# Performance work log

Measured on AMD Instinct MI355X. Metric: run time of the kernel, lower is better.

## Reference

```python
import jax, jax.numpy as jnp
import numpy as np
import math

B, TU, TM, D, H = 4, 2048, 256, 1024, 16
DH = D // H
PAIRS = D // 2
LAM = 0.7
EPS_PHASE = 1e-8


def balance_norm(x, w, b, bal_w):
    mu = x.mean(-1, keepdims=True)
    var = ((x - mu) ** 2).mean(-1, keepdims=True)
    normed = (x - mu) / jnp.sqrt(var + 1e-6) * w + b
    half = x.shape[-1] // 2
    e1 = (x[..., :half] ** 2).mean(-1, keepdims=True)
    e2 = (x[..., half:] ** 2).mean(-1, keepdims=True)
    imb = (e1 - e2) * bal_w  # (B,T,1)
    corr = jnp.concatenate([
        jnp.broadcast_to(-imb, x[..., :half].shape),
        jnp.broadcast_to(imb, x[..., half:].shape)], axis=-1)
    return normed + corr


def phase_resonance(a, b):
    # a: (B,Tq,D), b: (B,Tk,D). mean_p cos(th_a - th_b) == (cosA@cosB^T + sinA@sinB^T)/pairs
    def to_phase(x):
        x2 = x.reshape(*x.shape[:-1], PAIRS, 2)
        return jnp.arctan2(x2[..., 1] + EPS_PHASE, x2[..., 0] + EPS_PHASE)
    ta, tb = to_phase(a), to_phase(b)
    ca, sa = jnp.cos(ta), jnp.sin(ta)
    cb, sb = jnp.cos(tb), jnp.sin(tb)
    r = (jnp.einsum('bqp,bkp->bqk', ca, cb) + jnp.einsum('bqp,bkp->bqk', sa, sb)) / PAIRS
    return r


def mha(q_in, kv_in, wq, wk, wv, wo, a_gate, e_gate):
    Bq, Tq, _ = q_in.shape
    Tk = kv_in.shape[1]
    q = (q_in @ wq.T).reshape(Bq, Tq, H, DH)
    k = (kv_in @ wk.T).reshape(Bq, Tk, H, DH)
    v = (kv_in @ wv.T).reshape(Bq, Tk, H, DH)
    scores = jnp.einsum('bqhd,bkhd->bhqk', q, k) / math.sqrt(DH)
    attn = jax.nn.softmax(scores, axis=-1)
    ag = a_gate[:, None, :, :]              # (B,1,Tq,1)
    eg = jnp.swapaxes(e_gate[:, None], 2, 3)  # (B,1,1,Tk)
    attn = attn * ag * eg
    attn = attn / (attn.sum(-1, keepdims=True) + 1e-8)
    ctx = jnp.einsum('bhqk,bkhd->bqhd', attn, v).reshape(Bq, Tq, D)
    return ctx @ wo.T


def setup_inputs() -> dict:
    key = jax.random.key(0)
    ks = jax.random.split(key, 16)
    s = 0.02
    return {
        'o_micro': jax.random.normal(ks[0], (B, TU, D), jnp.float32),
        'o_macro': jax.random.normal(ks[1], (B, TM, D), jnp.float32),
        'r_conv_acc': jax.random.normal(ks[2], (B, TM, TU), jnp.float32) * 0.1,
        'r_emer_acc': jax.random.normal(ks[3], (B, TU, TM), jnp.float32) * 0.1,
        'ln_u_w': jnp.ones((D,), jnp.float32),
        'ln_u_b': jnp.zeros((D,), jnp.float32),
        'bw_u': jnp.float32(0.01),
        'ln_m_w': jnp.ones((D,), jnp.float32),
        'ln_m_b': jnp.zeros((D,), jnp.float32),
        'bw_m': jnp.float32(0.01),
        'gu_w': jax.random.normal(ks[4], (1, D), jnp.float32) * s,
        'gu_b': jnp.zeros((1,), jnp.float32),
        'gm_w': jax.random.normal(ks[5], (1, D), jnp.float32) * s,
        'gm_b': jnp.zeros((1,), jnp.float32),
        'conv_q_w': jax.random.normal(ks[6], (D, D), jnp.float32) * s,
        'conv_k_w': jax.random.normal(ks[7], (D, D), jnp.float32) * s,
        'conv_v_w': jax.random.normal(ks[8], (D, D), jnp.float32) * s,
        'conv_out_w': jax.random.normal(ks[9], (D, D), jnp.float32) * s,
        'emer_q_w': jax.random.normal(ks[10], (D, D), jnp.float32) * s,
        'emer_k_w': jax.random.normal(ks[11], (D, D), jnp.float32) * s,
        'emer_v_w': jax.random.normal(ks[12], (D, D), jnp.float32) * s,
        'emer_out_w': jax.random.normal(ks[13], (D, D), jnp.float32) * s,
        'res_alpha': jnp.float32(1.0),
    }


def reference(o_micro, o_macro, r_conv_acc, r_emer_acc,
              ln_u_w, ln_u_b, bw_u, ln_m_w, ln_m_b, bw_m,
              gu_w, gu_b, gm_w, gm_b,
              conv_q_w, conv_k_w, conv_v_w, conv_out_w,
              emer_q_w, emer_k_w, emer_v_w, emer_out_w, res_alpha):
    ou = balance_norm(o_micro, ln_u_w, ln_u_b, bw_u)
    om = balance_norm(o_macro, ln_m_w, ln_m_b, bw_m)
    g_micro = jax.nn.sigmoid(ou @ gu_w.T + gu_b)  # (B,Tu,1)
    g_macro = jax.nn.sigmoid(om @ gm_w.T + gm_b)  # (B,Tm,1)
    r_conv_inst = phase_resonance(om, ou)  # (B,Tm,Tu)
    r_emer_inst = phase_resonance(ou, om)  # (B,Tu,Tm)
    r_conv_new = LAM * r_conv_acc + (1 - LAM) * r_conv_inst
    r_emer_new = LAM * r_emer_acc + (1 - LAM) * r_emer_inst
    r_conv_scalar = jax.nn.sigmoid(res_alpha * r_conv_new.mean(-1, keepdims=True))
    r_emer_scalar = jax.nn.sigmoid(res_alpha * r_emer_new.mean(-1, keepdims=True))
    delta_macro = mha(om, ou, conv_q_w, conv_k_w, conv_v_w, conv_out_w, g_macro, g_micro)
    o_macro_new = o_macro + delta_macro * r_conv_scalar
    delta_micro = mha(ou, om, emer_q_w, emer_k_w, emer_v_w, emer_out_w, g_micro, g_macro)
    o_micro_new = o_micro + delta_micro * r_emer_scalar
    return (o_micro_new, o_macro_new, r_conv_new, r_emer_new)
```

## Files before the change

### kernel.cpp

```cpp
#include <hip/hip_runtime.h>
#include <math.h>

typedef unsigned short u16;
typedef __attribute__((ext_vector_type(8))) short bf16x8;
typedef __attribute__((ext_vector_type(4))) float f32x4;

__device__ __forceinline__ float sigmoidf_(float x) { return 1.0f / (1.0f + __expf(-x)); }
__device__ __forceinline__ u16 f2bf(float v) {
    union { float f; unsigned u; } x; x.f = v;
    unsigned r = x.u + 0x7fffu + ((x.u >> 16) & 1u);
    return (u16)(r >> 16);
}
__device__ __forceinline__ float bf2f(u16 u) {
    union { unsigned u; float f; } x; x.u = ((unsigned)u) << 16; return x.f;
}

#define GLD(src, dst) __builtin_amdgcn_global_load_lds( \
        (const __attribute__((address_space(1))) void*)(src), \
        (__attribute__((address_space(3))) void*)(dst), 16, 0, 0)
#define GLD4(src, dst) __builtin_amdgcn_global_load_lds( \
        (const __attribute__((address_space(1))) void*)(src), \
        (__attribute__((address_space(3))) void*)(dst), 4, 0, 0)

__global__ void __launch_bounds__(256) norm_gate_kernel(
    const float* __restrict__ X,
    const float* __restrict__ w, const float* __restrict__ bvec,
    const float* __restrict__ bw_p,
    const float* __restrict__ gw, const float* __restrict__ gb_p,
    u16* __restrict__ OUT, u16* __restrict__ PN, float* __restrict__ G)
{
    const int row = blockIdx.x * 4 + (threadIdx.x >> 6);
    const int lane = threadIdx.x & 63;
    const float* xr = X + (size_t)row * 1024 + lane * 16;
    float4 xa = ((const float4*)xr)[0];
    float4 xb = ((const float4*)xr)[1];
    float4 xc = ((const float4*)xr)[2];
    float4 xd = ((const float4*)xr)[3];
    float s1 = (xa.x + xa.y + xa.z + xa.w) + (xb.x + xb.y + xb.z + xb.w)
             + (xc.x + xc.y + xc.z + xc.w) + (xd.x + xd.y + xd.z + xd.w);
    float s2 = xa.x * xa.x + xa.y * xa.y + xa.z * xa.z + xa.w * xa.w
             + xb.x * xb.x + xb.y * xb.y + xb.z * xb.z + xb.w * xb.w
             + xc.x * xc.x + xc.y * xc.y + xc.z * xc.z + xc.w * xc.w
             + xd.x * xd.x + xd.y * xd.y + xd.z * xd.z + xd.w * xd.w;
    #pragma unroll
    for (int o = 1; o <= 32; o <<= 1) s1 += __shfl_xor(s1, o);
    float h2 = s2;
    #pragma unroll
    for (int o = 1; o <= 16; o <<= 1) h2 += __shfl_xor(h2, o);
    const float oth = __shfl_xor(h2, 32);
    const float slo = (lane < 32) ? h2 : oth;
    const float shi = (lane < 32) ? oth : h2;
    const float mu = s1 * (1.0f / 1024.0f);
    const float var = (slo + shi) * (1.0f / 1024.0f) - mu * mu;
    const float rstd = rsqrtf(var + 1e-6f);
    const float imb = (slo - shi) * (1.0f / 512.0f) * (*bw_p);
    const float corr = (lane < 32) ? -imb : imb;
    const int i0 = lane * 16;
    const float4* wp = (const float4*)(w + i0);
    const float4* bp = (const float4*)(bvec + i0);
    const float4* gp = (const float4*)(gw + i0);
    float o16[16];
    float gd = 0.0f;
    #pragma unroll
    for (int q = 0; q < 4; ++q) {
        float4 xv = (q == 0) ? xa : (q == 1) ? xb : (q == 2) ? xc : xd;
        float4 wv = wp[q], bv = bp[q], gv = gp[q];
        float t0 = (xv.x - mu) * rstd * wv.x + bv.x + corr;
        float t1 = (xv.y - mu) * rstd * wv.y + bv.y + corr;
        float t2 = (xv.z - mu) * rstd * wv.z + bv.z + corr;
        float t3 = (xv.w - mu) * rstd * wv.w + bv.w + corr;
        gd += t0 * gv.x + t1 * gv.y + t2 * gv.z + t3 * gv.w;
        o16[4 * q + 0] = t0; o16[4 * q + 1] = t1; o16[4 * q + 2] = t2; o16[4 * q + 3] = t3;
    }
    #pragma unroll
    for (int o = 1; o <= 32; o <<= 1) gd += __shfl_xor(gd, o);
    if (lane == 0) G[row] = sigmoidf_(gd + *gb_p);
    u16 ob[16], pn[16];
    #pragma unroll
    for (int j = 0; j < 16; ++j) ob[j] = f2bf(o16[j]);
    #pragma unroll
    for (int j = 0; j < 8; ++j) {
        float px = o16[2 * j] + 1e-8f, py = o16[2 * j + 1] + 1e-8f;
        float rr = rsqrtf(px * px + py * py);
        pn[2 * j] = f2bf(px * rr); pn[2 * j + 1] = f2bf(py * rr);
    }
    *(uint4*)(OUT + (size_t)row * 1024 + i0) = *(uint4*)ob;
    *(uint4*)(OUT + (size_t)row * 1024 + i0 + 8) = *(uint4*)(ob + 8);
    *(uint4*)(PN + (size_t)row * 1024 + i0) = *(uint4*)pn;
    *(uint4*)(PN + (size_t)row * 1024 + i0 + 8) = *(uint4*)(pn + 8);
}

__global__ void __launch_bounds__(256) wconv_kernel(
    const float* w0, const float* w1, const float* w2, const float* w3,
    const float* w4, const float* w5, const float* w6, const float* w7,
    u16* __restrict__ dst)
{
    const float* s;
    switch (blockIdx.y) {
        case 0: s = w0; break; case 1: s = w1; break;
        case 2: s = w2; break; case 3: s = w3; break;
        case 4: s = w4; break; case 5: s = w5; break;
        case 6: s = w6; break; default: s = w7; break;
    }
    long i = (long)blockIdx.x * 1024 + threadIdx.x * 4;
    float4 v = *(const float4*)(s + i);
    u16 o[4] = { f2bf(v.x), f2bf(v.y), f2bf(v.z), f2bf(v.w) };
    *(uint2*)(dst + (long)blockIdx.y * 1048576 + i) = *(uint2*)o;
}

__global__ void __launch_bounds__(256) attn_flash(
    const u16* __restrict__ Q, const u16* __restrict__ K,
    const u16* __restrict__ VT, const float* __restrict__ AG,
    const float* __restrict__ EG, u16* __restrict__ OC,
    int TQ, int TKV, long vbs)
{
    __shared__ __align__(16) u16 shm[21504];
    float* egf = (float*)(shm + 20480);
    const int t = threadIdx.x;
    const int lane = t & 63, w = t >> 6;
    const int l15 = lane & 15, g = lane >> 4;
    const int qt = blockIdx.x, h = blockIdx.y, b = blockIdx.z;
    const long qrow = (long)b * TQ + qt * 64 + w * 16 + l15;
    const u16* Qp = Q + qrow * 1024 + h * 64 + g * 8;
    const bf16x8 qf0 = *(const bf16x8*)(Qp);
    const bf16x8 qf1 = *(const bf16x8*)(Qp + 32);
    const u16* Kp = K + ((long)b * TKV + w * 16 + l15) * 1024 + h * 64 + g * 8;
    const u16* Vp = VT + (long)b * vbs + (long)(h * 64 + w * 16 + l15) * TKV + g * 8;
    const float* egp = EG + (long)b * TKV + lane;

    auto stage = [&](int kvt, int buf) {
        GLD(Kp + (long)kvt * 1024,      shm + buf * 4096 + (w * 2 + 0) * 512);
        GLD(Kp + (long)kvt * 1024 + 32, shm + buf * 4096 + (w * 2 + 1) * 512);
        GLD(Vp + kvt,      shm + 8192 + buf * 4096 + (w * 2 + 0) * 512);
        GLD(Vp + kvt + 32, shm + 8192 + buf * 4096 + (w * 2 + 1) * 512);
        GLD4(egp + kvt, egf + (buf * 4 + w) * 64);
    };

    const int nT = TKV >> 6;
    f32x4 O[4] = {};
    float mrun = -3.0e38f, lrun = 0.0f, serun = 0.0f;
    stage(0, 0);
    for (int i = 0; i < nT; ++i) {
        const int buf = i & 1;
        if (i + 1 < nT) {
            stage((i + 1) << 6, buf ^ 1);
            asm volatile("s_waitcnt vmcnt(5)" ::: "memory");
        } else {
            asm volatile("s_waitcnt vmcnt(0)" ::: "memory");
        }
        __builtin_amdgcn_sched_barrier(0);
        __builtin_amdgcn_s_barrier();
        const u16* kb = shm + buf * 4096;
        const u16* vb = shm + 8192 + buf * 4096;
        f32x4 sa[4] = {};
        #pragma unroll
        for (int kvf = 0; kvf < 4; ++kvf) {
            bf16x8 kf = *(const bf16x8*)(kb + (kvf * 2 + 0) * 512 + lane * 8);
            sa[kvf] = __builtin_amdgcn_mfma_f32_16x16x32_bf16(kf, qf0, sa[kvf], 0, 0, 0);
        }
        #pragma unroll
        for (int kvf = 0; kvf < 4; ++kvf) {
            bf16x8 kf = *(const bf16x8*)(kb + (kvf * 2 + 1) * 512 + lane * 8);
            sa[kvf] = __builtin_amdgcn_mfma_f32_16x16x32_bf16(kf, qf1, sa[kvf], 0, 0, 0);
        }
        float ev[4][4];
        float tmax = -3.0e38f;
        #pragma unroll
        for (int kvf = 0; kvf < 4; ++kvf)
            #pragma unroll
            for (int j = 0; j < 4; ++j) {
                float s = sa[kvf][j] * 0.125f;
                ev[kvf][j] = s;
                tmax = fmaxf(tmax, s);
            }
        tmax = fmaxf(tmax, __shfl_xor(tmax, 16));
        tmax = fmaxf(tmax, __shfl_xor(tmax, 32));
        const float mnew = fmaxf(mrun, tmax);
        const float corr = __expf(mrun - mnew);
        mrun = mnew;
        float suml = 0.0f, sumg = 0.0f;
        unsigned pk[4][2];
        #pragma unroll
        for (int kvf = 0; kvf < 4; ++kvf) {
            float4 eg4 = *(const float4*)(egf + (buf * 4 + w) * 64 + kvf * 16 + 4 * g);
            float e0 = __expf(ev[kvf][0] - mnew);
            float e1 = __expf(ev[kvf][1] - mnew);
            float e2 = __expf(ev[kvf][2] - mnew);
            float e3 = __expf(ev[kvf][3] - mnew);
            suml += (e0 + e1) + (e2 + e3);
            float g0 = e0 * eg4.x, g1 = e1 * eg4.y, g2 = e2 * eg4.z, g3 = e3 * eg4.w;
            sumg += (g0 + g1) + (g2 + g3);
            pk[kvf][0] = (unsigned)f2bf(g0) | ((unsigned)f2bf(g1) << 16);
            pk[kvf][1] = (unsigned)f2bf(g2) | ((unsigned)f2bf(g3) << 16);
        }
        suml += __shfl_xor(suml, 16); suml += __shfl_xor(suml, 32);
        sumg += __shfl_xor(sumg, 16); sumg += __shfl_xor(sumg, 32);
        lrun = lrun * corr + suml;
        serun = serun * corr + sumg;
        #pragma unroll
        for (int fd = 0; fd < 4; ++fd)
            #pragma unroll
            for (int j = 0; j < 4; ++j) O[fd][j] *= corr;
        u16* pw = shm + 16384 + w * 1024;
        #pragma unroll
        for (int kvf = 0; kvf < 4; ++kvf) {
            const int base = (kvf >> 1) * 512
                           + (l15 + 16 * (2 * (kvf & 1) + (g >> 1))) * 8
                           + 4 * (g & 1);
            *(unsigned*)(pw + base) = pk[kvf][0];
            *(unsigned*)(pw + base + 2) = pk[kvf][1];
        }
        #pragma unroll
        for (int ksv = 0; ksv < 2; ++ksv) {
            bf16x8 pf = *(const bf16x8*)(pw + ksv * 512 + lane * 8);
            #pragma unroll
            for (int fd = 0; fd < 4; ++fd) {
                bf16x8 vf = *(const bf16x8*)(vb + (fd * 2 + ksv) * 512 + lane * 8);
                O[fd] = __builtin_amdgcn_mfma_f32_16x16x32_bf16(vf, pf, O[fd], 0, 0, 0);
            }
        }
        if (i + 1 < nT) __builtin_amdgcn_s_barrier();
    }
    const float agv = AG[qrow];
    const float fac = agv / (agv * serun + lrun * 1e-8f);
    __syncthreads();
    u16* tw = shm + w * 1152;
    #pragma unroll
    for (int fd = 0; fd < 4; ++fd) {
        const int d0 = fd * 16 + 4 * g;
        unsigned v01 = (unsigned)f2bf(O[fd][0] * fac) | ((unsigned)f2bf(O[fd][1] * fac) << 16);
        unsigned v23 = (unsigned)f2bf(O[fd][2] * fac) | ((unsigned)f2bf(O[fd][3] * fac) << 16);
        *(unsigned*)(tw + l15 * 72 + d0) = v01;
        *(unsigned*)(tw + l15 * 72 + d0 + 2) = v23;
    }
    const int qr = lane >> 2, part = lane & 3;
    uint4 va = *(const uint4*)(tw + qr * 72 + part * 16);
    uint4 vb2 = *(const uint4*)(tw + qr * 72 + part * 16 + 8);
    u16* op = OC + ((long)b * TQ + qt * 64 + w * 16 + qr) * 1024 + h * 64 + part * 16;
    *(uint4*)(op) = va;
    *(uint4*)(op + 8) = vb2;
}

#define RD_A(BUF, MQ) do { \
    _Pragma("unroll") for (int fr_ = 0; fr_ < 4; ++fr_) \
    _Pragma("unroll") for (int kk_ = 0; kk_ < 2; ++kk_) \
        af[fr_][kk_] = *(const bf16x8*)(sh + (BUF) * BUFSZ + (MQ) * 8192 + (wm * 4 + fr_) * 1024 + kk_ * 512 + lane * 8); \
} while (0)
#define RD_B(BUF, NQ, DST) do { \
    _Pragma("unroll") for (int fc_ = 0; fc_ < NRC; ++fc_) \
    _Pragma("unroll") for (int kk_ = 0; kk_ < 2; ++kk_) \
        DST[fc_][kk_] = *(const bf16x8*)(sh + (BUF) * BUFSZ + 16384 + (NQ) * BHALF + (wn * NRC + fc_) * 1024 + kk_ * 512 + lane * 8); \
} while (0)
#define MM(SRC, MQ, NQ) do { \
    __builtin_amdgcn_s_setprio(1); \
    _Pragma("unroll") for (int fr_ = 0; fr_ < 4; ++fr_) \
    _Pragma("unroll") for (int fc_ = 0; fc_ < NRC; ++fc_) \
    _Pragma("unroll") for (int kk_ = 0; kk_ < 2; ++kk_) \
        acc[(MQ) * 4 + fr_][(NQ) * NRC + fc_] = __builtin_amdgcn_mfma_f32_16x16x32_bf16( \
            af[fr_][kk_], SRC[fc_][kk_], acc[(MQ) * 4 + fr_][(NQ) * NRC + fc_], 0, 0, 0); \
    __builtin_amdgcn_s_setprio(0); \
} while (0)
#define FENCE1() do { \
    __builtin_amdgcn_s_barrier(); \
    asm volatile("s_waitcnt lgkmcnt(0)" ::: "memory"); \
    __builtin_amdgcn_sched_barrier(0); \
} while (0)
#define FENCE2(VM) do { \
    __builtin_amdgcn_sched_barrier(0); \
    if ((VM) == 1) { \
        if constexpr (BN == 256) asm volatile("s_waitcnt vmcnt(8)" ::: "memory"); \
        else                     asm volatile("s_waitcnt vmcnt(6)" ::: "memory"); \
    } else if ((VM) == 2) { asm volatile("s_waitcnt vmcnt(0)" ::: "memory"); } \
    __builtin_amdgcn_s_barrier(); \
} while (0)

template<int BN, int EPI>
__global__ void __launch_bounds__(512, 1) mfma256(
    const u16* __restrict__ A, const u16* __restrict__ B,
    void* __restrict__ C, void* __restrict__ Cx, void* __restrict__ Cy,
    int K, int lda, int ldb,
    const float* __restrict__ base, const float* __restrict__ rs)
{
    constexpr int NRC = BN / 128;
    constexpr int BHALF = BN * 32;
    constexpr int BUFSZ = 16384 + 2 * BHALF;
    extern __shared__ u16 sh[];
    const int gx = gridDim.x, gy = gridDim.y;
    const int lin = blockIdx.x + gx * blockIdx.y;
    const int xcd = lin & 7, off = lin >> 3;
    const int lby = gy >> 3;
    const int by = xcd * lby + (off % lby);
    const int bx = off / lby;
    const int t = threadIdx.x;
    const int lane = t & 63, w = t >> 6;
    const int wm = w >> 2, wn = w & 3;
    const long m0 = (long)by * 256;
    const long n0 = (long)bx * BN;
    const int l15 = lane & 15, g = lane >> 4;

    auto stageA = [&](int h, int kt, int buf) {
        const long kb = (long)kt * 64 + g * 8;
        #pragma unroll
        for (int r2 = 0; r2 < 2; ++r2) {
            const int c = w + 8 * r2;
            const int sub = c >> 1, kc = c & 1;
            GLD(A + (m0 + h * 128 + sub * 16 + l15) * lda + kb + kc * 32,
                sh + buf * BUFSZ + h * 8192 + c * 512);
        }
    };
    auto stageB = [&](int h, int kt, int buf) {
        const long kb = (long)kt * 64 + g * 8;
        if constexpr (BN == 256) {
            #pragma unroll
            for (int r2 = 0; r2 < 2; ++r2) {
                const int c = w + 8 * r2;
                const int sub = c >> 1, kc = c & 1;
                GLD(B + (n0 + h * 128 + sub * 16 + l15) * ldb + kb + kc * 32,
                    sh + buf * BUFSZ + 16384 + h * BHALF + c * 512);
            }
        } else {
            const int c = w;
            const int sub = c >> 1, kc = c & 1;
            GLD(B + (n0 + h * 64 + sub * 16 + l15) * ldb + kb + kc * 32,
                sh + buf * BUFSZ + 16384 + h * BHALF + c * 512);
        }
    };

    const int nIter = K >> 7;
    f32x4 acc[8][2 * NRC] = {};
    bf16x8 af[4][2], bf0[NRC][2], bf1[NRC][2];

    stageA(0, 0, 0); stageA(1, 0, 0); stageB(0, 0, 0); stageB(1, 0, 0);
    stageA(0, 1, 1); stageA(1, 1, 1); stageB(0, 1, 1); stageB(1, 1, 1);
    if constexpr (BN == 256) asm volatile("s_waitcnt vmcnt(8)" ::: "memory");
    else                     asm volatile("s_waitcnt vmcnt(6)" ::: "memory");
    __builtin_amdgcn_sched_barrier(0);
    __builtin_amdgcn_s_barrier();

    for (int i = 0; i < nIter; ++i) {
        const bool pre = (i + 1 < nIter);
        const int ktA = 2 * i + 2, ktB = 2 * i + 3;
        RD_A(0, 0); RD_B(0, 0, bf0);
        FENCE1(); MM(bf0, 0, 0); FENCE2(0);
        RD_B(0, 1, bf1);
        if (pre) { stageA(0, ktA, 0); stageB(0, ktA, 0); }
        FENCE1(); MM(bf1, 0, 1); FENCE2(0);
        RD_A(0, 1);
        if (pre) stageB(1, ktA, 0);
        FENCE1(); MM(bf1, 1, 1); FENCE2(0);
        if (pre) stageA(1, ktA, 0);
        FENCE1(); MM(bf0, 1, 0); FENCE2(pre ? 1 : 2);
        RD_A(1, 0); RD_B(1, 0, bf0);
        FENCE1(); MM(bf0, 0, 0); FENCE2(0);
        RD_B(1, 1, bf1);
        if (pre) { stageA(0, ktB, 1); stageB(0, ktB, 1); }
        FENCE1(); MM(bf1, 0, 1); FENCE2(0);
        RD_A(1, 1);
        if (pre) stageB(1, ktB, 1);
        FENCE1(); MM(bf1, 1, 1); FENCE2(0);
        if (pre) stageA(1, ktB, 1);
        FENCE1(); MM(bf0, 1, 0); FENCE2(pre ? 1 : 0);
    }

    #pragma unroll
    for (int mq = 0; mq < 2; ++mq)
    #pragma unroll
    for (int fr = 0; fr < 4; ++fr)
    #pragma unroll
    for (int nq = 0; nq < 2; ++nq)
    #pragma unroll
    for (int fc = 0; fc < NRC; ++fc) {
        const long grow0 = m0 + mq * 128 + wm * 64 + fr * 16 + g * 4;
        const long gcol = n0 + nq * (BN / 2) + wn * (16 * NRC) + fc * 16 + l15;
        const f32x4 a = acc[mq * 4 + fr][nq * NRC + fc];
        if constexpr (EPI == 3) {
            #pragma unroll
            for (int j = 0; j < 4; ++j) {
                const long idx = (grow0 + j) * 1024 + gcol;
                ((float*)C)[idx] = base[idx] + a[j] * rs[grow0 + j];
            }
        } else {
            const int sec = (int)(n0 >> 10);
            if (sec == 0) {
                #pragma unroll
                for (int j = 0; j < 4; ++j)
                    ((u16*)C)[(grow0 + j) * 1024 + gcol] = f2bf(a[j]);
            } else if (sec == 1) {
                const long col = gcol - 1024;
                u16 pk[4] = { f2bf(a[0]), f2bf(a[1]), f2bf(a[2]), f2bf(a[3]) };
                const long idx = (grow0 >> 11) * 2097152 + col * 2048 + (grow0 & 2047);
                *(uint2*)&((u16*)Cx)[idx] = *(uint2*)pk;
            } else {
                #pragma unroll
                for (int j = 0; j < 4; ++j)
                    ((u16*)Cy)[(grow0 + j) * 1024 + (gcol - 2048)] = f2bf(a[j]);
            }
        }
    }
}
#undef RD_A
#undef RD_B
#undef MM
#undef FENCE1
#undef FENCE2

template<int BN, int EPI, bool SWZ>
__global__ void __launch_bounds__(256) mfma_nt(
    const u16* __restrict__ A, long zAb, long zAh,
    const u16* __restrict__ B, long zBb, long zBh,
    void* __restrict__ C, long zCb, long zCh,
    void* __restrict__ Cx, void* __restrict__ Cy,
    int K, int lda, int ldb, int ldc, float alpha, int nH, int nsplit,
    const float* __restrict__ base, const float* __restrict__ rs,
    const float* __restrict__ accB, float* __restrict__ OT,
    long zOT, int ldt)
{
    constexpr int NR = BN / 32;
    constexpr int ABUF = 128 * 32;
    constexpr int BBUF = BN * 32;
    __shared__ __align__(16) u16 sh[3 * (ABUF + BBUF)];
    u16* const Ab0 = sh;
    u16* const Bb0 = sh + 3 * ABUF;
    int bx, by, bz;
    if constexpr (SWZ) {
        const int gx = gridDim.x, gy = gridDim.y;
        const int lin = blockIdx.x + gx * blockIdx.y;
        const int xcd = lin & 7, c = lin >> 3;
        const int LBY = gy >> 3;
        const int SPB = 4 * LBY;
        const int sc = c / SPB, rr = c - sc * SPB;
        const int byl = rr >> 2, bxl = rr & 3;
        by = xcd * LBY + byl;
        bx = sc * 4 + bxl;
        bz = 0;
    } else {
        bx = blockIdx.x; by = blockIdx.y; bz = blockIdx.z;
    }
    const int t = threadIdx.x;
    const int lane = t & 63, w = t >> 6;
    const int wr = w >> 1, wc = w & 1;
    const int slab = bz / nsplit, ks = bz - slab * nsplit;
    const int b = slab / nH, h = slab - b * nH;
    const int kchunk = K / nsplit;
    const int kbeg = ks * kchunk, kend = kbeg + kchunk;
    const long m0 = (long)by * 128;
    const long n0 = (long)bx * BN;
    const int frow = lane & 15, fko = (lane >> 4) * 8;
    const u16* gaA = A + zAb * b + zAh * h + (m0 + 32 * w + frow) * lda + fko;
    const u16* gbB;
    if constexpr (BN == 128) gbB = B + zBb * b + zBh * h + (n0 + 32 * w + frow) * ldb + fko;
    else                     gbB = B + zBb * b + zBh * h + (n0 + 16 * w + frow) * ldb + fko;

    auto stage = [&](int kk, int p) {
        u16* ap = Ab0 + p * ABUF;
        u16* bp = Bb0 + p * BBUF;
        GLD(gaA + kk, ap + 2 * w * 512);
        GLD(gaA + 16L * lda + kk, ap + (2 * w + 1) * 512);
        if constexpr (BN == 128) {
            GLD(gbB + kk, bp + 2 * w * 512);
            GLD(gbB + 16L * ldb + kk, bp + (2 * w + 1) * 512);
        } else {
            GLD(gbB + kk, bp + w * 512);
        }
    };

    const int nIter = (kend - kbeg) >> 5;
    f32x4 acc[4][NR] = {};
    stage(kbeg, 0);
    if (nIter > 1) stage(kbeg + 32, 1);
    int cur = 0;
    for (int i = 0; i < nIter; ++i) {
        if (i + 2 < nIter) {
            int p2 = cur + 2; if (p2 >= 3) p2 -= 3;
            stage(kbeg + (i + 2) * 32, p2);
            if constexpr (BN == 128) asm volatile("s_waitcnt vmcnt(8)" ::: "memory");
            else                     asm volatile("s_waitcnt vmcnt(6)" ::: "memory");
        } else if (i + 1 < nIter) {
            if constexpr (BN == 128) asm volatile("s_waitcnt vmcnt(4)" ::: "memory");
            else                     asm volatile("s_waitcnt vmcnt(3)" ::: "memory");
        } else {
            asm volatile("s_waitcnt vmcnt(0)" ::: "memory");
        }
        __builtin_amdgcn_sched_barrier(0);
        __builtin_amdgcn_s_barrier();
        __builtin_amdgcn_sched_barrier(0);
        const u16* ap = Ab0 + cur * ABUF;
        const u16* bp = Bb0 + cur * BBUF;
        bf16x8 af[4], bfr[NR];
        #pragma unroll
        for (int m = 0; m < 4; ++m)
            af[m] = *(const bf16x8*)(ap + (wr * 4 + m) * 512 + lane * 8);
        #pragma unroll
        for (int n = 0; n < NR; ++n)
            bfr[n] = *(const bf16x8*)(bp + (wc * NR + n) * 512 + lane * 8);
        asm volatile("s_waitcnt lgkmcnt(0)" ::: "memory");
        __builtin_amdgcn_sched_barrier(0);
        __builtin_amdgcn_s_barrier();
        #pragma unroll
        for (int m = 0; m < 4; ++m)
            #pragma unroll
            for (int n = 0; n < NR; ++n)
                acc[m][n] = __builtin_amdgcn_mfma_f32_16x16x32_bf16(af[m], bfr[n], acc[m][n], 0, 0, 0);
        cur = (cur == 2) ? 0 : cur + 1;
    }
    const long Coff = zCb * b + zCh * h;
    const int l15 = lane & 15, l4 = lane >> 4;
    #pragma unroll
    for (int m = 0; m < 4; ++m) {
        #pragma unroll
        for (int n = 0; n < NR; ++n) {
            #pragma unroll
            for (int j = 0; j < 4; ++j) {
                const long grow = m0 + wr * 64 + m * 16 + l4 * 4 + j;
                const long gcol = n0 + wc * (BN / 2) + n * 16 + l15;
                const float v = acc[m][n][j] * alpha;
                if constexpr (EPI == 3) {
                    const long idx = grow * ldc + gcol;
                    ((float*)C)[idx] = base[idx] + v * rs[grow];
                } else if constexpr (EPI == 5) {
                    const long idx = Coff + grow * ldc + gcol;
                    ((float*)C)[idx] = 0.7f * base[idx] + 0.3f * v;
                    const long tidx = zOT * b + gcol * (long)ldt + grow;
                    OT[tidx] = 0.7f * accB[tidx] + 0.3f * v;
                } else if constexpr (EPI == 7) {
                    const int sec = (int)(n0 >> 10);
                    if (sec == 0) ((u16*)C)[grow * 1024 + gcol] = f2bf(v);
                    else if (sec == 1) ((u16*)Cx)[grow * 1024 + (gcol - 1024)] = f2bf(v);
                    else {
                        const long col = gcol - 2048;
                        ((u16*)Cy)[(grow >> 8) * 262144 + col * 256 + (grow & 255)] = f2bf(v);
                    }
                }
            }
        }
    }
}

__global__ void __launch_bounds__(256) rowmean_sig_kernel(
    const float* __restrict__ X, int len, float invlen,
    const float* __restrict__ alpha_p, float* __restrict__ OUT)
{
    const int row = blockIdx.x * 4 + (threadIdx.x >> 6);
    const int lane = threadIdx.x & 63;
    const float* xr = X + (long)row * len;
    float s = 0.0f;
    for (int k = lane; k < len; k += 64) s += xr[k];
    for (int o = 32; o > 0; o >>= 1) s += __shfl_xor(s, o);
    if (lane == 0) OUT[row] = sigmoidf_((*alpha_p) * s * invlen);
}

#define MFMA_TAIL nullptr, nullptr, nullptr, nullptr, 0L, 0

extern "C" void kernel_launch(void* const* d_in, const int* in_sizes, int n_in,
                              void* d_out, int out_size, void* d_ws, size_t ws_size,
                              hipStream_t stream)
{
    (void)in_sizes; (void)n_in; (void)out_size; (void)ws_size;
    const float* o_micro    = (const float*)d_in[0];
    const float* o_macro    = (const float*)d_in[1];
    const float* r_conv_acc = (const float*)d_in[2];
    const float* r_emer_acc = (const float*)d_in[3];
    const float* ln_u_w = (const float*)d_in[4];
    const float* ln_u_b = (const float*)d_in[5];
    const float* bw_u   = (const float*)d_in[6];
    const float* ln_m_w = (const float*)d_in[7];
    const float* ln_m_b = (const float*)d_in[8];
    const float* bw_m   = (const float*)d_in[9];
    const float* gu_w   = (const float*)d_in[10];
    const float* gu_b   = (const float*)d_in[11];
    const float* gm_w   = (const float*)d_in[12];
    const float* gm_b   = (const float*)d_in[13];
    const float* wq_c   = (const float*)d_in[14];
    const float* wk_c   = (const float*)d_in[15];
    const float* wv_c   = (const float*)d_in[16];
    const float* wo_c   = (const float*)d_in[17];
    const float* wq_e   = (const float*)d_in[18];
    const float* wk_e   = (const float*)d_in[19];
    const float* wv_e   = (const float*)d_in[20];
    const float* wo_e   = (const float*)d_in[21];
    const float* res_alpha = (const float*)d_in[22];

    float* out = (float*)d_out;
    float* out_micro = out;
    float* out_macro = out + 8388608;
    float* out_rconv = out + 9437184;
    float* out_remer = out + 11534336;

    float* ws = (float*)d_ws;
    u16* OUb = (u16*)ws;
    u16* OMb = (u16*)(ws + 4194304);
    u16* WB  = (u16*)(ws + 4718592);
    u16* Kcb = (u16*)(ws + 8912896);
    u16* VTc = (u16*)(ws + 13107200);
    u16* Qeb = (u16*)(ws + 17301504);
    u16* Qcb = (u16*)(ws + 21495808);
    u16* Keb = (u16*)(ws + 22020096);
    u16* VTe = (u16*)(ws + 22544384);
    u16* PNu = (u16*)(ws + 23068672);
    float* CT = ws + 27262976;
    float* GU = ws + 28311552;
    float* GM = GU + 8192;
    float* RCS = GM + 1024;
    float* RES = RCS + 1024;
    u16* PNm = (u16*)CT;
    u16* CTc = (u16*)CT;
    u16* CTe = Kcb;

    wconv_kernel<<<dim3(1024, 8), 256, 0, stream>>>(wk_c, wv_c, wq_e, wq_c, wk_e, wv_e, wo_c, wo_e, WB);
    norm_gate_kernel<<<2048, 256, 0, stream>>>(o_micro, ln_u_w, ln_u_b, bw_u, gu_w, gu_b, OUb, PNu, GU);
    norm_gate_kernel<<<256, 256, 0, stream>>>(o_macro, ln_m_w, ln_m_b, bw_m, gm_w, gm_b, OMb, PNm, GM);
    mfma_nt<128, 5, false><<<dim3(16, 2, 4), 256, 0, stream>>>(
        PNm, 262144L, 0L, PNu, 2097152L, 0L, out_rconv, 524288L, 0L, nullptr, nullptr,
        1024, 1024, 1024, 2048, 1.0f / 512.0f, 1, 1,
        r_conv_acc, nullptr, r_emer_acc, out_remer, 524288L, 256);
    rowmean_sig_kernel<<<256, 256, 0, stream>>>(out_rconv, 2048, 1.0f / 2048.0f, res_alpha, RCS);
    rowmean_sig_kernel<<<2048, 256, 0, stream>>>(out_remer, 256, 1.0f / 256.0f, res_alpha, RES);
    mfma256<256, 6><<<dim3(12, 32), 512, 131072, stream>>>(
        OUb, WB, Kcb, VTc, Qeb, 1024, 1024, 1024, nullptr, nullptr);
    mfma_nt<128, 7, true><<<dim3(24, 8, 1), 256, 0, stream>>>(
        OMb, 0L, 0L, WB + 3 * 1048576, 0L, 0L, Qcb, 0L, 0L, Keb, VTe,
        1024, 1024, 1024, 1024, 1.0f, 1, 1, MFMA_TAIL);
    attn_flash<<<dim3(4, 16, 4), 256, 0, stream>>>(
        Qcb, Kcb, VTc, GM, GU, CTc, 256, 2048, 2097152L);
    mfma_nt<128, 3, false><<<dim3(8, 8, 1), 256, 0, stream>>>(
        CTc, 0L, 0L, WB + 6 * 1048576, 0L, 0L, out_macro, 0L, 0L, nullptr, nullptr,
        1024, 1024, 1024, 1024, 1.0f, 1, 1, o_macro, RCS, nullptr, nullptr, 0L, 0);
    attn_flash<<<dim3(32, 16, 4), 256, 0, stream>>>(
        Qeb, Keb, VTe, GU, GM, CTe, 2048, 256, 262144L);
    mfma256<128, 3><<<dim3(8, 32), 512, 98304, stream>>>(
        CTe, WB + 7 * 1048576, out_micro, nullptr, nullptr,
        1024, 1024, 1024, o_micro, RES);
}
```

Measured before the change: 299.2 us.

## Stage transposed resonance output through LDS and switch micro out-proj GEMM kernel

The phase-resonance GEMM epilogue used to write the transposed r_emer output with strided scalar stores. It now stages the accumulator tile in shared memory and writes coalesced float4 rows, blending with the accumulator input. This adds extra barriers and reuses the LDS buffer. Separately, the final micro output projection now uses the mfma_nt 128-tile kernel on an 8x64 grid instead of the mfma256 kernel, which changes occupancy and tiling.

Measured after the change: 305.2 us. +2.0%, slower.

```diff
diff --git a/kernel.cpp b/kernel.cpp
--- a/kernel.cpp
+++ b/kernel.cpp
@@ -520,8 +520,6 @@
                 } else if constexpr (EPI == 5) {
                     const long idx = Coff + grow * ldc + gcol;
                     ((float*)C)[idx] = 0.7f * base[idx] + 0.3f * v;
-                    const long tidx = zOT * b + gcol * (long)ldt + grow;
-                    OT[tidx] = 0.7f * accB[tidx] + 0.3f * v;
                 } else if constexpr (EPI == 7) {
                     const int sec = (int)(n0 >> 10);
                     if (sec == 0) ((u16*)C)[grow * 1024 + gcol] = f2bf(v);
@@ -532,6 +530,40 @@
                     }
                 }
             }
+        }
+    }
+    if constexpr (EPI == 5) {
+        float* tf = (float*)sh;
+        __syncthreads();
+        #pragma unroll
+        for (int h2 = 0; h2 < 2; ++h2) {
+            if (wc == h2) {
+                #pragma unroll
+                for (int m = 0; m < 4; ++m)
+                    #pragma unroll
+                    for (int n = 0; n < NR; ++n)
+                        #pragma unroll
+                        for (int j = 0; j < 4; ++j)
+                            tf[(n * 16 + l15) * 132 + wr * 64 + m * 16 + l4 * 4 + j]
+                                = alpha * acc[m][n][j];
+            }
+            __syncthreads();
+            const int r0 = t >> 5, q4 = (t & 31) * 4;
+            #pragma unroll
+            for (int ri = 0; ri < 8; ++ri) {
+                const int row = r0 + 8 * ri;
+                const long kglob = n0 + h2 * 64 + row;
+                const long obase = zOT * b + kglob * (long)ldt + m0 + q4;
+                float4 v4 = *(float4*)&tf[row * 132 + q4];
+                float4 a4 = *(const float4*)&accB[obase];
+                float4 o4;
+                o4.x = 0.7f * a4.x + 0.3f * v4.x;
+                o4.y = 0.7f * a4.y + 0.3f * v4.y;
+                o4.z = 0.7f * a4.z + 0.3f * v4.z;
+                o4.w = 0.7f * a4.w + 0.3f * v4.w;
+                *(float4*)&OT[obase] = o4;
+            }
+            if (h2 == 0) __syncthreads();
         }
     }
 }
@@ -627,7 +659,7 @@
         1024, 1024, 1024, 1024, 1.0f, 1, 1, o_macro, RCS, nullptr, nullptr, 0L, 0);
     attn_flash<<<dim3(32, 16, 4), 256, 0, stream>>>(
         Qeb, Keb, VTe, GU, GM, CTe, 2048, 256, 262144L);
-    mfma256<128, 3><<<dim3(8, 32), 512, 98304, stream>>>(
-        CTe, WB + 7 * 1048576, out_micro, nullptr, nullptr,
-        1024, 1024, 1024, o_micro, RES);
-}
+    mfma_nt<128, 3, true><<<dim3(8, 64, 1), 256, 0, stream>>>(
+        CTe, 0L, 0L, WB + 7 * 1048576, 0L, 0L, out_micro, 0L, 0L, nullptr, nullptr,
+        1024, 1024, 1024, 1024, 1.0f, 1, 1, o_micro, RES, nullptr, nullptr, 0L, 0);
+}
```
